# Optimization experiments

Measured on AMD Instinct MI355X. Metric: run time of the kernel, lower is better.

The kernel has to match this reference:

```python
import jax, jax.numpy as jnp
import numpy as np

B, S, D, E, H, TOPK = 4, 2048, 1024, 32, 128, 4

def setup_inputs() -> dict:
    key = jax.random.key(0)
    k1, k2, k3, k4 = jax.random.split(key, 4)
    x = jax.random.normal(k1, (B, S, D), jnp.float32)
    expert_sel = jax.random.normal(k2, (E, D), jnp.float32) * (D ** -0.5)
    keys = jax.random.normal(k3, (E, D, H), jnp.float32) * (D ** -0.5)
    values = jax.random.normal(k4, (E, H, D), jnp.float32) * (H ** -0.5)
    return {"x": x, "expert_sel": expert_sel, "keys": keys, "values": values, "n_heads": TOPK}

def reference(x, expert_sel, keys, values, n_heads):
    # x: [B,S,D]; expert_sel: [E,D]; keys: [E,D,H]; values: [E,H,D]
    Bv, Sv, Dv = x.shape
    Ev = keys.shape[0]
    xf = x.reshape(-1, Dv)                                  # [N,D]
    N = xf.shape[0]
    gate = jax.nn.sigmoid(xf @ expert_sel.T)                # [N,E] sigmoid gating (sigma-MoE)
    vals, idx = jax.lax.top_k(gate, n_heads)                # [N,k] selected experts + gate weights
    # dense per-token-per-expert gate weights; zero for non-selected experts
    g = jnp.zeros((N, Ev), x.dtype).at[jnp.arange(N)[:, None], idx].set(vals)  # [N,E]
    # grouped expert FFN, expressed densely over the (small) expert axis:
    # out = sum_e g[n,e] * relu(x @ keys[e]) @ values[e]
    h = jax.nn.relu(jnp.einsum('nd,edh->enh', xf, keys))    # [E,N,H]
    out = jnp.einsum('enh,ehd->nd', h * g.T[:, :, None], values)  # [N,D]
    return out.reshape(Bv, Sv, Dv)
```

## Files before the change

### kernel.cpp

```cpp
#include <hip/hip_runtime.h>
#include <hip/hip_bf16.h>

#define NTOK 8192
#define DDIM 1024
#define NEXP 32
#define HDIM 128
#define TOPK 4

typedef __attribute__((ext_vector_type(8))) short bf16x8;
typedef __attribute__((ext_vector_type(4))) float f32x4;

typedef unsigned int uint_g __attribute__((address_space(1)));
typedef unsigned int uint_l __attribute__((address_space(3)));

__device__ __forceinline__ void async_cp16(const void* g, void* l) {
    __builtin_amdgcn_global_load_lds((const uint_g*)g, (uint_l*)l, 16, 0, 0);
}

__device__ inline unsigned short f2bf(float f) {
    unsigned int u = __builtin_bit_cast(unsigned int, f);
    unsigned int r = (u + 0x7fffu + ((u >> 16) & 1u)) >> 16;
    return (unsigned short)r;
}
__device__ inline float bf2f(unsigned short s) {
    unsigned int u = ((unsigned int)s) << 16;
    return __builtin_bit_cast(float, u);
}

__global__ __launch_bounds__(256) void prep_weights(
    const float* __restrict__ x,
    const float* __restrict__ keys, const float* __restrict__ values,
    unsigned short* __restrict__ Kb, unsigned short* __restrict__ Vb,
    unsigned short* __restrict__ Xb)
{
    int idx = blockIdx.x * 256 + threadIdx.x;
    unsigned short o[8];
    if (idx < NEXP * 128 * 128) {
        int n = idx & 127, k0 = (idx >> 7) & 127, e = idx >> 14;
        const float* s = keys + ((size_t)e * DDIM + k0 * 8) * HDIM + n;
        #pragma unroll
        for (int j = 0; j < 8; ++j) o[j] = f2bf(s[(size_t)j * HDIM]);
        *(uint4*)&Kb[(size_t)idx * 8] = *(uint4*)o;
    } else if (idx < 2 * NEXP * 128 * 128) {
        idx -= NEXP * 128 * 128;
        int n = idx & 1023, k0 = (idx >> 10) & 15, e = idx >> 14;
        const float* s = values + ((size_t)e * HDIM + k0 * 8) * DDIM + n;
        #pragma unroll
        for (int j = 0; j < 8; ++j) o[j] = f2bf(s[(size_t)j * DDIM]);
        *(uint4*)&Vb[(size_t)idx * 8] = *(uint4*)o;
    } else {
        idx -= 2 * NEXP * 128 * 128;
        const float* s = x + (size_t)idx * 8;
        #pragma unroll
        for (int j = 0; j < 8; ++j) o[j] = f2bf(s[j]);
        *(uint4*)&Xb[(size_t)idx * 8] = *(uint4*)o;
    }
}

__global__ __launch_bounds__(256) void gate_partial(
    const float* __restrict__ x, const float* __restrict__ es,
    float* __restrict__ gpart)
{
    const int n0    = blockIdx.x * 16;
    const int dbase = blockIdx.y * 256;
    const int tid   = threadIdx.x;

    __shared__ float smem[4608];
    float* Xt  = smem;
    float* Est = smem + 64 * 36;

    const int t4  = (tid & 3) * 4;
    const int e4  = ((tid >> 2) & 7) * 4;
    const int rep = tid >> 5;

    const int xr = tid & 15, xc4 = (tid >> 4) * 4;
    const int er = tid & 31, ec8 = (tid >> 5) * 8;

    float acc[4][4] = {};

    for (int dc = dbase; dc < dbase + 256; dc += 64) {
        __syncthreads();
        {
            float4 v = *(const float4*)&x[(size_t)(n0 + xr) * DDIM + dc + xc4];
            Xt[(xc4 + 0) * 36 + xr] = v.x; Xt[(xc4 + 1) * 36 + xr] = v.y;
            Xt[(xc4 + 2) * 36 + xr] = v.z; Xt[(xc4 + 3) * 36 + xr] = v.w;
        }
        #pragma unroll
        for (int i = 0; i < 2; ++i) {
            float4 v = *(const float4*)&es[(size_t)er * DDIM + dc + ec8 + i * 4];
            Est[(ec8 + i * 4 + 0) * 36 + er] = v.x;
            Est[(ec8 + i * 4 + 1) * 36 + er] = v.y;
            Est[(ec8 + i * 4 + 2) * 36 + er] = v.z;
            Est[(ec8 + i * 4 + 3) * 36 + er] = v.w;
        }
        __syncthreads();

        #pragma unroll
        for (int s = 0; s < 8; ++s) {
            int d = s * 8 + rep;
            float4 xv = *(const float4*)&Xt[d * 36 + t4];
            float4 ev = *(const float4*)&Est[d * 36 + e4];
            const float xa[4] = {xv.x, xv.y, xv.z, xv.w};
            const float ea[4] = {ev.x, ev.y, ev.z, ev.w};
            #pragma unroll
            for (int i = 0; i < 4; ++i)
                #pragma unroll
                for (int j = 0; j < 4; ++j)
                    acc[i][j] = fmaf(xa[i], ea[j], acc[i][j]);
        }
    }

    __syncthreads();
    float* Lp = smem;
    #pragma unroll
    for (int i = 0; i < 4; ++i)
        #pragma unroll
        for (int j = 0; j < 4; ++j)
            Lp[(rep * 16 + t4 + i) * 33 + e4 + j] = acc[i][j];
    __syncthreads();

    for (int p = tid; p < 16 * 32; p += 256) {
        int tok = p >> 5, e = p & 31;
        float s = 0.f;
        #pragma unroll
        for (int r = 0; r < 8; ++r) s += Lp[(r * 16 + tok) * 33 + e];
        gpart[((size_t)blockIdx.y * NTOK + n0 + tok) * NEXP + e] = s;
    }
}

__global__ __launch_bounds__(256) void topk_scatter(
    const float* __restrict__ gpart,
    int* __restrict__ cnt, int* __restrict__ tok_list, float* __restrict__ gates)
{
    const int tid = threadIdx.x;
    const int n   = blockIdx.x * 256 + tid;

    __shared__ int hist[NEXP];
    __shared__ int bbase[NEXP];
    if (tid < NEXP) hist[tid] = 0;

    float lg[NEXP];
    #pragma unroll
    for (int i = 0; i < 8; ++i) {
        float4 v = *(const float4*)&gpart[(size_t)n * NEXP + i * 4];
        lg[i*4+0] = v.x; lg[i*4+1] = v.y; lg[i*4+2] = v.z; lg[i*4+3] = v.w;
    }
    #pragma unroll
    for (int j = 1; j < 4; ++j)
        #pragma unroll
        for (int i = 0; i < 8; ++i) {
            float4 v = *(const float4*)&gpart[((size_t)j * NTOK + n) * NEXP + i * 4];
            lg[i*4+0] += v.x; lg[i*4+1] += v.y; lg[i*4+2] += v.z; lg[i*4+3] += v.w;
        }

    int sel[TOPK]; float sv[TOPK];
    #pragma unroll
    for (int j = 0; j < TOPK; ++j) {
        float bv = -3.0e38f; int bi = 0;
        #pragma unroll
        for (int e = 0; e < NEXP; ++e) {
            bool taken = false;
            #pragma unroll
            for (int q = 0; q < j; ++q) taken = taken || (sel[q] == e);
            float v = taken ? -3.0e38f : lg[e];
            if (v > bv) { bv = v; bi = e; }
        }
        sel[j] = bi; sv[j] = bv;
    }

    __syncthreads();
    int lpos[TOPK];
    #pragma unroll
    for (int j = 0; j < TOPK; ++j) {
        gates[n * TOPK + j] = 1.f / (1.f + expf(-sv[j]));
        lpos[j] = atomicAdd(&hist[sel[j]], 1);
    }
    __syncthreads();
    if (tid < NEXP) bbase[tid] = atomicAdd(&cnt[tid], hist[tid]);
    __syncthreads();
    #pragma unroll
    for (int j = 0; j < TOPK; ++j)
        tok_list[(size_t)sel[j] * NTOK + bbase[sel[j]] + lpos[j]] = n * TOPK + j;
}

__global__ __launch_bounds__(256) void ffn_phase1(
    const unsigned short* __restrict__ Xb,
    const unsigned short* __restrict__ Kb,
    const int* __restrict__ cnt, const int* __restrict__ tok_list,
    const float* __restrict__ gates,
    unsigned short* __restrict__ Hb)
{
    const int e = blockIdx.y, tile = blockIdx.x;
    const int c = cnt[e], base = tile * 32;
    if (base >= c) return;
    const int nt   = min(32, c - base);
    const int tid  = threadIdx.x, wave = tid >> 6, lane = tid & 63;
    const int lm   = lane & 15, quad = lane >> 4;
    const int r2   = (wave >> 1) * 16, c2 = (wave & 1) * 64;

    __shared__ __align__(16) unsigned short Ks[8192];
    __shared__ __align__(16) unsigned short Xs[2048];
    __shared__ int slot[32]; __shared__ int gtok[32]; __shared__ float gs[32];

    if (tid < 32) {
        if (tid < nt) {
            int v = tok_list[(size_t)e * NTOK + base + tid];
            slot[tid] = v; gtok[tid] = v >> 2; gs[tid] = gates[v];
        } else { slot[tid] = -1; gtok[tid] = 0; gs[tid] = 0.f; }
    }
    __syncthreads();

    const unsigned short* Ke   = Kb + (size_t)e * 131072;
    const unsigned short* xrow = Xb + (size_t)gtok[lane & 31] * DDIM + (lane >> 5) * 8;

    f32x4 acc[4];
    #pragma unroll
    for (int j = 0; j < 4; ++j) acc[j] = (f32x4){0.f, 0.f, 0.f, 0.f};

    auto stage = [&](int t) {
        int dc = t * 64;
        #pragma unroll
        for (int i = 0; i < 4; ++i) {
            int p = wave * 4 + i;
            async_cp16(Ke + ((size_t)(dc / 8 + (p >> 1)) * 128 + (p & 1) * 64 + lane) * 8,
                       &Ks[p * 512]);
        }
        if (wave == 0) {
            #pragma unroll
            for (int p = 0; p < 4; ++p)
                async_cp16(xrow + dc + p * 16, &Xs[p * 512]);
        }
    };

    stage(0);
    __syncthreads();

    for (int t = 0; t < 16; ++t) {
        #pragma unroll
        for (int ks = 0; ks < 2; ++ks) {
            int k0 = ks * 4 + quad;
            bf16x8 a = *(const bf16x8*)&Xs[(k0 * 32 + r2 + lm) * 8];
            #pragma unroll
            for (int tj = 0; tj < 4; ++tj) {
                bf16x8 bb = *(const bf16x8*)&Ks[(k0 * 128 + c2 + tj * 16 + lm) * 8];
                acc[tj] = __builtin_amdgcn_mfma_f32_16x16x32_bf16(a, bb, acc[tj], 0, 0, 0);
            }
        }
        if (t < 15) {
            __syncthreads();
            stage(t + 1);
            __syncthreads();
        }
    }

    #pragma unroll
    for (int reg = 0; reg < 4; ++reg) {
        int m = r2 + quad * 4 + reg;
        int s = slot[m];
        if (s >= 0) {
            float g = gs[m];
            unsigned short* hp = Hb + (size_t)s * HDIM;
            #pragma unroll
            for (int tj = 0; tj < 4; ++tj)
                hp[c2 + tj * 16 + lm] = f2bf(fmaxf(acc[tj][reg], 0.f) * g);
        }
    }
}

__global__ __launch_bounds__(256) void ffn_phase2(
    const unsigned short* __restrict__ Hb,
    const unsigned short* __restrict__ Vb,
    const int* __restrict__ cnt, const int* __restrict__ tok_list,
    unsigned short* __restrict__ Ob)
{
    const int e = blockIdx.y, tile = blockIdx.x;
    const int c = cnt[e], base = tile * 32;
    if (base >= c) return;
    const int nt   = min(32, c - base);
    const int tid  = threadIdx.x, wave = tid >> 6, lane = tid & 63;
    const int lm   = lane & 15, quad = lane >> 4;
    const int r2   = (wave >> 1) * 16, cw = (wave & 1) * 32;

    __shared__ __align__(16) unsigned short Hs[4096];
    __shared__ __align__(16) unsigned short Vs[8192];
    __shared__ int slot[32];

    if (tid < 32)
        slot[tid] = (tid < nt) ? tok_list[(size_t)e * NTOK + base + tid] : -1;
    __syncthreads();

    const unsigned short* Ve = Vb + (size_t)e * 131072;
    int gl = slot[lane & 31]; if (gl < 0) gl = 0;
    const unsigned short* hrow = Hb + (size_t)gl * HDIM + (lane >> 5) * 8;

    auto stageV = [&](int cc) {
        #pragma unroll
        for (int i = 0; i < 4; ++i) {
            int p = wave * 4 + i;
            async_cp16(Ve + ((size_t)p * 1024 + cc * 64 + lane) * 8, &Vs[p * 512]);
        }
    };

    if (wave == 0) {
        #pragma unroll
        for (int p = 0; p < 8; ++p)
            async_cp16(hrow + p * 16, &Hs[p * 512]);
    }
    stageV(0);
    __syncthreads();

    for (int cc = 0; cc < 16; ++cc) {
        f32x4 acc[2];
        acc[0] = (f32x4){0.f, 0.f, 0.f, 0.f};
        acc[1] = (f32x4){0.f, 0.f, 0.f, 0.f};

        #pragma unroll
        for (int ks = 0; ks < 4; ++ks) {
            int k0 = ks * 4 + quad;
            bf16x8 a = *(const bf16x8*)&Hs[(k0 * 32 + r2 + lm) * 8];
            #pragma unroll
            for (int tj = 0; tj < 2; ++tj) {
                bf16x8 bb = *(const bf16x8*)&Vs[(k0 * 64 + cw + tj * 16 + lm) * 8];
                acc[tj] = __builtin_amdgcn_mfma_f32_16x16x32_bf16(a, bb, acc[tj], 0, 0, 0);
            }
        }

        #pragma unroll
        for (int reg = 0; reg < 4; ++reg) {
            int m = r2 + quad * 4 + reg;
            int s = slot[m];
            if (s >= 0) {
                unsigned short* op = Ob + (size_t)s * DDIM + cc * 64 + cw + lm;
                op[0]  = f2bf(acc[0][reg]);
                op[16] = f2bf(acc[1][reg]);
            }
        }

        if (cc < 15) {
            __syncthreads();
            stageV(cc + 1);
            __syncthreads();
        }
    }
}

__global__ __launch_bounds__(256) void reduce_out(
    const unsigned short* __restrict__ Ob, float* __restrict__ out)
{
    const int tid = threadIdx.x;
    const int n   = blockIdx.x * 2 + (tid >> 7);
    const int cc  = (tid & 127) * 8;

    float s[8] = {};
    #pragma unroll
    for (int j = 0; j < 4; ++j) {
        uint4 v = *(const uint4*)&Ob[((size_t)n * 4 + j) * DDIM + cc];
        const unsigned int w[4] = {v.x, v.y, v.z, v.w};
        #pragma unroll
        for (int q = 0; q < 4; ++q) {
            s[q * 2 + 0] += bf2f((unsigned short)(w[q] & 0xffff));
            s[q * 2 + 1] += bf2f((unsigned short)(w[q] >> 16));
        }
    }
    float4 o0 = {s[0], s[1], s[2], s[3]};
    float4 o1 = {s[4], s[5], s[6], s[7]};
    *(float4*)&out[(size_t)n * DDIM + cc]     = o0;
    *(float4*)&out[(size_t)n * DDIM + cc + 4] = o1;
}

extern "C" void kernel_launch(void* const* d_in, const int* in_sizes, int n_in,
                              void* d_out, int out_size, void* d_ws, size_t ws_size,
                              hipStream_t stream) {
    const float* x      = (const float*)d_in[0];
    const float* es     = (const float*)d_in[1];
    const float* keys   = (const float*)d_in[2];
    const float* values = (const float*)d_in[3];
    float* out          = (float*)d_out;

    char* w = (char*)d_ws;
    int*   cnt      = (int*)w;               w += 256;
    int*   tok_list = (int*)w;               w += (size_t)NEXP * NTOK * sizeof(int);
    float* gates    = (float*)w;             w += (size_t)NTOK * TOPK * sizeof(float);
    float* gpart    = (float*)w;             w += (size_t)4 * NTOK * NEXP * sizeof(float);
    unsigned short* Kb = (unsigned short*)w; w += (size_t)NEXP * 128 * 128 * 8 * 2;
    unsigned short* Vb = (unsigned short*)w; w += (size_t)NEXP * 16 * 1024 * 8 * 2;
    unsigned short* Hb = (unsigned short*)w; w += (size_t)NTOK * TOPK * HDIM * 2;
    unsigned short* Ob = (unsigned short*)w;
    unsigned short* Xb = Ob;

    hipMemsetAsync(cnt, 0, NEXP * sizeof(int), stream);

    prep_weights<<<8192, 256, 0, stream>>>(x, keys, values, Kb, Vb, Xb);
    gate_partial<<<dim3(NTOK / 16, 4), 256, 0, stream>>>(x, es, gpart);
    topk_scatter<<<NTOK / 256, 256, 0, stream>>>(gpart, cnt, tok_list, gates);

    ffn_phase1<<<dim3(128, NEXP), 256, 0, stream>>>(Xb, Kb, cnt, tok_list, gates, Hb);
    ffn_phase2<<<dim3(128, NEXP), 256, 0, stream>>>(Hb, Vb, cnt, tok_list, Ob);
    reduce_out<<<NTOK / 2, 256, 0, stream>>>(Ob, out);
}
```

Baseline: 223.4 us.

## Fuse expert FFN phases into one kernel keeping hidden activations in LDS

Merges the two expert FFN kernels into a single kernel. The gated ReLU hidden tile is written to a padded LDS buffer instead of global memory, and is then consumed directly by the value projection. The K and V staging buffers share one LDS region. This removes one kernel launch plus the global write and re-read of the hidden activations. In exchange it uses more LDS per block and serialises both GEMMs within each block. Xb now gets its own workspace region because Ob is written while Xb is still being read.

```diff
diff --git a/kernel.cpp b/kernel.cpp
--- a/kernel.cpp
+++ b/kernel.cpp
@@ -183,12 +183,13 @@
         tok_list[(size_t)sel[j] * NTOK + bbase[sel[j]] + lpos[j]] = n * TOPK + j;
 }
 
-__global__ __launch_bounds__(256) void ffn_phase1(
+__global__ __launch_bounds__(256) void ffn_fused(
     const unsigned short* __restrict__ Xb,
     const unsigned short* __restrict__ Kb,
+    const unsigned short* __restrict__ Vb,
     const int* __restrict__ cnt, const int* __restrict__ tok_list,
     const float* __restrict__ gates,
-    unsigned short* __restrict__ Hb)
+    unsigned short* __restrict__ Ob)
 {
     const int e = blockIdx.y, tile = blockIdx.x;
     const int c = cnt[e], base = tile * 32;
@@ -196,10 +197,13 @@
     const int nt   = min(32, c - base);
     const int tid  = threadIdx.x, wave = tid >> 6, lane = tid & 63;
     const int lm   = lane & 15, quad = lane >> 4;
-    const int r2   = (wave >> 1) * 16, c2 = (wave & 1) * 64;
-
-    __shared__ __align__(16) unsigned short Ks[8192];
+    const int r2   = (wave >> 1) * 16;
+    const int c2   = (wave & 1) * 64;
+    const int cw   = (wave & 1) * 32;
+
+    __shared__ __align__(16) unsigned short KV[8192];
     __shared__ __align__(16) unsigned short Xs[2048];
+    __shared__ __align__(16) unsigned short Hs[32 * 136];
     __shared__ int slot[32]; __shared__ int gtok[32]; __shared__ float gs[32];
 
     if (tid < 32) {
@@ -211,19 +215,20 @@
     __syncthreads();
 
     const unsigned short* Ke   = Kb + (size_t)e * 131072;
+    const unsigned short* Ve   = Vb + (size_t)e * 131072;
     const unsigned short* xrow = Xb + (size_t)gtok[lane & 31] * DDIM + (lane >> 5) * 8;
 
     f32x4 acc[4];
     #pragma unroll
     for (int j = 0; j < 4; ++j) acc[j] = (f32x4){0.f, 0.f, 0.f, 0.f};
 
-    auto stage = [&](int t) {
+    auto stageA = [&](int t) {
         int dc = t * 64;
         #pragma unroll
         for (int i = 0; i < 4; ++i) {
             int p = wave * 4 + i;
             async_cp16(Ke + ((size_t)(dc / 8 + (p >> 1)) * 128 + (p & 1) * 64 + lane) * 8,
-                       &Ks[p * 512]);
+                       &KV[p * 512]);
         }
         if (wave == 0) {
             #pragma unroll
@@ -232,7 +237,7 @@
         }
     };
 
-    stage(0);
+    stageA(0);
     __syncthreads();
 
     for (int t = 0; t < 16; ++t) {
@@ -242,13 +247,13 @@
             bf16x8 a = *(const bf16x8*)&Xs[(k0 * 32 + r2 + lm) * 8];
             #pragma unroll
             for (int tj = 0; tj < 4; ++tj) {
-                bf16x8 bb = *(const bf16x8*)&Ks[(k0 * 128 + c2 + tj * 16 + lm) * 8];
+                bf16x8 bb = *(const bf16x8*)&KV[(k0 * 128 + c2 + tj * 16 + lm) * 8];
                 acc[tj] = __builtin_amdgcn_mfma_f32_16x16x32_bf16(a, bb, acc[tj], 0, 0, 0);
             }
         }
         if (t < 15) {
             __syncthreads();
-            stage(t + 1);
+            stageA(t + 1);
             __syncthreads();
         }
     }
@@ -256,72 +261,37 @@
     #pragma unroll
     for (int reg = 0; reg < 4; ++reg) {
         int m = r2 + quad * 4 + reg;
-        int s = slot[m];
-        if (s >= 0) {
-            float g = gs[m];
-            unsigned short* hp = Hb + (size_t)s * HDIM;
-            #pragma unroll
-            for (int tj = 0; tj < 4; ++tj)
-                hp[c2 + tj * 16 + lm] = f2bf(fmaxf(acc[tj][reg], 0.f) * g);
-        }
-    }
-}
-
-__global__ __launch_bounds__(256) void ffn_phase2(
-    const unsigned short* __restrict__ Hb,
-    const unsigned short* __restrict__ Vb,
-    const int* __restrict__ cnt, const int* __restrict__ tok_list,
-    unsigned short* __restrict__ Ob)
-{
-    const int e = blockIdx.y, tile = blockIdx.x;
-    const int c = cnt[e], base = tile * 32;
-    if (base >= c) return;
-    const int nt   = min(32, c - base);
-    const int tid  = threadIdx.x, wave = tid >> 6, lane = tid & 63;
-    const int lm   = lane & 15, quad = lane >> 4;
-    const int r2   = (wave >> 1) * 16, cw = (wave & 1) * 32;
-
-    __shared__ __align__(16) unsigned short Hs[4096];
-    __shared__ __align__(16) unsigned short Vs[8192];
-    __shared__ int slot[32];
-
-    if (tid < 32)
-        slot[tid] = (tid < nt) ? tok_list[(size_t)e * NTOK + base + tid] : -1;
-    __syncthreads();
-
-    const unsigned short* Ve = Vb + (size_t)e * 131072;
-    int gl = slot[lane & 31]; if (gl < 0) gl = 0;
-    const unsigned short* hrow = Hb + (size_t)gl * HDIM + (lane >> 5) * 8;
+        float g = gs[m];
+        #pragma unroll
+        for (int tj = 0; tj < 4; ++tj)
+            Hs[m * 136 + c2 + tj * 16 + lm] = f2bf(fmaxf(acc[tj][reg], 0.f) * g);
+    }
+    __syncthreads();
 
     auto stageV = [&](int cc) {
         #pragma unroll
         for (int i = 0; i < 4; ++i) {
             int p = wave * 4 + i;
-            async_cp16(Ve + ((size_t)p * 1024 + cc * 64 + lane) * 8, &Vs[p * 512]);
+            async_cp16(Ve + ((size_t)p * 1024 + cc * 64 + lane) * 8, &KV[p * 512]);
         }
     };
 
-    if (wave == 0) {
-        #pragma unroll
-        for (int p = 0; p < 8; ++p)
-            async_cp16(hrow + p * 16, &Hs[p * 512]);
-    }
     stageV(0);
     __syncthreads();
 
     for (int cc = 0; cc < 16; ++cc) {
-        f32x4 acc[2];
-        acc[0] = (f32x4){0.f, 0.f, 0.f, 0.f};
-        acc[1] = (f32x4){0.f, 0.f, 0.f, 0.f};
+        f32x4 acc2[2];
+        acc2[0] = (f32x4){0.f, 0.f, 0.f, 0.f};
+        acc2[1] = (f32x4){0.f, 0.f, 0.f, 0.f};
 
         #pragma unroll
         for (int ks = 0; ks < 4; ++ks) {
             int k0 = ks * 4 + quad;
-            bf16x8 a = *(const bf16x8*)&Hs[(k0 * 32 + r2 + lm) * 8];
+            bf16x8 a = *(const bf16x8*)&Hs[(r2 + lm) * 136 + k0 * 8];
             #pragma unroll
             for (int tj = 0; tj < 2; ++tj) {
-                bf16x8 bb = *(const bf16x8*)&Vs[(k0 * 64 + cw + tj * 16 + lm) * 8];
-                acc[tj] = __builtin_amdgcn_mfma_f32_16x16x32_bf16(a, bb, acc[tj], 0, 0, 0);
+                bf16x8 bb = *(const bf16x8*)&KV[(k0 * 64 + cw + tj * 16 + lm) * 8];
+                acc2[tj] = __builtin_amdgcn_mfma_f32_16x16x32_bf16(a, bb, acc2[tj], 0, 0, 0);
             }
         }
 
@@ -331,8 +301,8 @@
             int s = slot[m];
             if (s >= 0) {
                 unsigned short* op = Ob + (size_t)s * DDIM + cc * 64 + cw + lm;
-                op[0]  = f2bf(acc[0][reg]);
-                op[16] = f2bf(acc[1][reg]);
+                op[0]  = f2bf(acc2[0][reg]);
+                op[16] = f2bf(acc2[1][reg]);
             }
         }
 
@@ -384,9 +354,8 @@
     float* gpart    = (float*)w;             w += (size_t)4 * NTOK * NEXP * sizeof(float);
     unsigned short* Kb = (unsigned short*)w; w += (size_t)NEXP * 128 * 128 * 8 * 2;
     unsigned short* Vb = (unsigned short*)w; w += (size_t)NEXP * 16 * 1024 * 8 * 2;
-    unsigned short* Hb = (unsigned short*)w; w += (size_t)NTOK * TOPK * HDIM * 2;
+    unsigned short* Xb = (unsigned short*)w; w += (size_t)NTOK * DDIM * 2;
     unsigned short* Ob = (unsigned short*)w;
-    unsigned short* Xb = Ob;
 
     hipMemsetAsync(cnt, 0, NEXP * sizeof(int), stream);
 
@@ -394,7 +363,6 @@
     gate_partial<<<dim3(NTOK / 16, 4), 256, 0, stream>>>(x, es, gpart);
     topk_scatter<<<NTOK / 256, 256, 0, stream>>>(gpart, cnt, tok_list, gates);
 
-    ffn_phase1<<<dim3(128, NEXP), 256, 0, stream>>>(Xb, Kb, cnt, tok_list, gates, Hb);
-    ffn_phase2<<<dim3(128, NEXP), 256, 0, stream>>>(Hb, Vb, cnt, tok_list, Ob);
+    ffn_fused<<<dim3(128, NEXP), 256, 0, stream>>>(Xb, Kb, Vb, cnt, tok_list, gates, Ob);
     reduce_out<<<NTOK / 2, 256, 0, stream>>>(Ob, out);
 }
```

New measurement: 225.3 us. No clear change (+0.8%).
